# Kernel tuning notes

Measured on AMD Instinct MI355X. Metric: run time of the kernel, lower is better.

## Reference

```python
import jax, jax.numpy as jnp
import numpy as np

BLOCK_SIZE = 1024
DILATIONS = (1, 2, 4, 8)


def setup_inputs() -> dict:
    key = jax.random.key(0)
    kq, kk, kv, kw, kb = jax.random.split(key, 5)
    b, h, L, hd = 4, 8, 4096, 64
    hidden = h * hd
    return {
        "query_states": jax.random.normal(kq, (b, h, L, hd), jnp.float32),
        "key_states": jax.random.normal(kk, (b, h, L, hd), jnp.float32),
        "value_states": jax.random.normal(kv, (b, h, L, hd), jnp.float32),
        "Wo": jax.random.normal(kw, (hidden, hidden), jnp.float32),
        "bo": jax.random.normal(kb, (hidden,), jnp.float32),
    }


def _dilated_branch(q, k, v, d):
    """One dilation pass: strided gather -> block attention.
    Returns de (bsz, nh, Ld, 1) detached exp-row-sums and a (bsz, nh, Ld, hd)."""
    b, h, L, hd = q.shape
    qs, ks, vs = q[:, :, ::d], k[:, :, ::d], v[:, :, ::d]
    Ld = qs.shape[2]
    bs = min(BLOCK_SIZE, Ld)          # torch.split: one short block if Ld < block_size
    nb = Ld // bs                      # even split for chosen q_len
    blk = lambda x: x.reshape(b, h, nb, bs, hd)
    qb, kb, vb = blk(qs), blk(ks), blk(vs)
    scores = jnp.einsum('bhnqd,bhnkd->bhnqk', qb, kb) / jnp.sqrt(jnp.float32(hd))
    # detached, unstabilized exp-sum (matches attn_weights.detach().exp().sum(-1))
    de = jax.lax.stop_gradient(jnp.exp(scores).sum(-1, keepdims=True)).reshape(b, h, Ld, 1)
    probs = jax.nn.softmax(scores.astype(jnp.float32), axis=-1).astype(q.dtype)
    a = jnp.einsum('bhnqk,bhnkd->bhnqd', probs, vb).reshape(b, h, Ld, hd)
    return de, a


def reference(query_states, key_states, value_states, Wo, bo):
    b, h, L, hd = query_states.shape
    w = jnp.zeros((b, h, L, 1), jnp.float32)
    des, rs = [], []
    for d in DILATIONS:
        de, a = _dilated_branch(query_states, key_states, value_states, d)
        des.append(de)
        rs.append(a)
        w = w.at[:, :, ::d].add(de)
    out = jnp.zeros_like(query_states)
    for d, de, a in zip(DILATIONS, des, rs):
        aw = de / w[:, :, ::d]                     # (b, h, Ld, 1) relative weight
        out = out.at[:, :, ::d].add((aw * a).astype(query_states.dtype))
    out = out.transpose(0, 2, 1, 3).reshape(b, L, h * hd)
    return out @ Wo.T + bo
```

## Files before the change

### kernel.cpp

```cpp
#include <hip/hip_runtime.h>
#include <hip/hip_bf16.h>

typedef __attribute__((ext_vector_type(8))) short bf16x8;
typedef __attribute__((ext_vector_type(4))) float f32x4;
typedef unsigned short u16;

union F8 { bf16x8 v; unsigned u[4]; u16 s[8]; uint4 q; };

__device__ __forceinline__ unsigned pk2(float a, float b) {
    __hip_bfloat162 t = __float22bfloat162_rn(make_float2(a, b));
    unsigned r; __builtin_memcpy(&r, &t, 4); return r;
}
__device__ __forceinline__ u16 f2bf(float a) {
    __hip_bfloat16 t = __float2bfloat16(a);
    u16 r; __builtin_memcpy(&r, &t, 2); return r;
}
__device__ __forceinline__ float bf2f(u16 s) {
    unsigned u = ((unsigned)s) << 16; float f; __builtin_memcpy(&f, &u, 4); return f;
}
#define SWZ(byteoff, row) ((byteoff) ^ (((row) & 7) << 4))
#define MFMA(a, b, c) __builtin_amdgcn_mfma_f32_16x16x32_bf16((a), (b), (c), 0, 0, 0)

__global__ __launch_bounds__(256)
void prep_kernel(const float* __restrict__ K, const float* __restrict__ V,
                 u16* __restrict__ Kb, u16* __restrict__ Vt)
{
    __shared__ __align__(16) char tl[64 * 128];
    int blk = blockIdx.x;
    const int t = threadIdx.x;

    if (blk < 2048) {
        const int bh = blk >> 6, qt = blk & 63;
        const int q = qt * 64 + (t >> 2), dd0 = (t & 3) * 16;
        const float* kp = K + ((size_t)bh * 4096 + q) * 64 + dd0;
        float4 x0 = ((const float4*)kp)[0], x1 = ((const float4*)kp)[1];
        float4 x2 = ((const float4*)kp)[2], x3 = ((const float4*)kp)[3];
        F8 f0, f1;
        f0.u[0] = pk2(x0.x, x0.y); f0.u[1] = pk2(x0.z, x0.w);
        f0.u[2] = pk2(x1.x, x1.y); f0.u[3] = pk2(x1.z, x1.w);
        f1.u[0] = pk2(x2.x, x2.y); f1.u[1] = pk2(x2.z, x2.w);
        f1.u[2] = pk2(x3.x, x3.y); f1.u[3] = pk2(x3.z, x3.w);
        u16* op = Kb + ((size_t)bh * 4096 + q) * 64 + dd0;
        ((uint4*)op)[0] = f0.q; ((uint4*)op)[1] = f1.q;
        return;
    }
    blk -= 2048;
    int d, Ld; size_t vtoff;
    if (blk < 2048)      { d = 1; Ld = 4096; vtoff = 0; }
    else if (blk < 3072) { blk -= 2048; d = 2; Ld = 2048; vtoff = 8388608; }
    else if (blk < 3584) { blk -= 3072; d = 4; Ld = 1024; vtoff = 12582912; }
    else                 { blk -= 3584; d = 8; Ld = 512;  vtoff = 14680064; }
    const int tpb = Ld >> 6;
    const int bh = blk / tpb, jt = blk % tpb;
    {
        const int j = t >> 2, dd0 = (t & 3) * 16;
        const int q = (jt * 64 + j) * d;
        const float* vp = V + ((size_t)bh * 4096 + q) * 64 + dd0;
        float4 x0 = ((const float4*)vp)[0], x1 = ((const float4*)vp)[1];
        float4 x2 = ((const float4*)vp)[2], x3 = ((const float4*)vp)[3];
        F8 f0, f1;
        f0.u[0] = pk2(x0.x, x0.y); f0.u[1] = pk2(x0.z, x0.w);
        f0.u[2] = pk2(x1.x, x1.y); f0.u[3] = pk2(x1.z, x1.w);
        f1.u[0] = pk2(x2.x, x2.y); f1.u[1] = pk2(x2.z, x2.w);
        f1.u[2] = pk2(x3.x, x3.y); f1.u[3] = pk2(x3.z, x3.w);
        *(uint4*)(tl + SWZ(j * 128 + dd0 * 2, j)) = f0.q;
        *(uint4*)(tl + SWZ(j * 128 + dd0 * 2 + 16, j)) = f1.q;
    }
    __syncthreads();
    {
        const int dd = t >> 2, jb = (t & 3) * 16;
        F8 f0, f1;
#pragma unroll
        for (int i = 0; i < 8; ++i) {
            f0.s[i] = *(const u16*)(tl + SWZ((jb + i) * 128 + dd * 2, jb + i));
            f1.s[i] = *(const u16*)(tl + SWZ((jb + 8 + i) * 128 + dd * 2, jb + 8 + i));
        }
        u16* op = Vt + vtoff + ((size_t)bh * 64 + dd) * Ld + jt * 64 + jb;
        ((uint4*)op)[0] = f0.q; ((uint4*)op)[1] = f1.q;
    }
}

__global__ __launch_bounds__(256)
void attn_fused(const float* __restrict__ Q, const u16* __restrict__ Kb,
                const u16* __restrict__ Vt, float* __restrict__ num,
                float* __restrict__ wsum, int phase)
{
    const int L = 4096;
    const int per = gridDim.x >> 3;
    const int wg0 = blockIdx.x;
    const int wg = (wg0 & 7) * per + (wg0 >> 3);

    int d, npb, bs, rel; size_t vtoff;
    if (phase == 0)     { d = 1; npb = 32; bs = 1024; rel = wg;       vtoff = 0; }
    else if (wg < 512)  { d = 2; npb = 16; bs = 1024; rel = wg;       vtoff = 8388608; }
    else if (wg < 768)  { d = 4; npb = 8;  bs = 1024; rel = wg - 512; vtoff = 12582912; }
    else                { d = 8; npb = 4;  bs = 512;  rel = wg - 768; vtoff = 14680064; }

    const int bh = rel / npb;
    const int qt = rel % npb;
    const int b = bh >> 3, h = bh & 7;
    const int tid = threadIdx.x;
    const int w = tid >> 6, lane = tid & 63;
    const int g = lane >> 4, c = lane & 15;
    const int bstart = ((qt * 128) / bs) * bs;
    const int qrow0 = qt * 128 + w * 32;
    const int Ldq = npb * 128;
    const int nt = bs >> 6;

    __shared__ __align__(16) char smem[32 * 1024];
    char* const Kls = smem;
    char* const Vls = smem + 8192;
    char* const Pls = smem + 16384 + w * 4096;

    const size_t base = (size_t)bh * L * 64;
    const size_t vbase = vtoff + (size_t)bh * 64 * Ldq;
    const float qs = 0.125f * 1.44269504088896341f;

    bf16x8 qf[2][2];
#pragma unroll
    for (int qi = 0; qi < 2; ++qi) {
        const float* qp = Q + base + (size_t)(qrow0 + qi * 16 + c) * d * 64 + g * 8;
#pragma unroll
        for (int s2 = 0; s2 < 2; ++s2) {
            float4 x = ((const float4*)(qp + s2 * 32))[0];
            float4 y = ((const float4*)(qp + s2 * 32))[1];
            F8 f;
            f.u[0] = pk2(x.x * qs, x.y * qs);
            f.u[1] = pk2(x.z * qs, x.w * qs);
            f.u[2] = pk2(y.x * qs, y.y * qs);
            f.u[3] = pk2(y.z * qs, y.w * qs);
            qf[qi][s2] = f.v;
        }
    }

    f32x4 o[2][4];
#pragma unroll
    for (int qi = 0; qi < 2; ++qi)
#pragma unroll
        for (int dj = 0; dj < 4; ++dj) o[qi][dj] = (f32x4){0.f, 0.f, 0.f, 0.f};
    float lrow[2] = {0.f, 0.f};

    const int krow = tid >> 2, kc = tid & 3;

    uint4 ka, kb2, va, vb;
    const u16* kp0 = Kb + base + (size_t)(bstart + krow) * d * 64 + kc * 16;
    const u16* vp0 = Vt + vbase + (size_t)lane * Ldq + bstart + w * 16;
    const size_t kstep = (size_t)64 * d * 64;
    ka = ((const uint4*)kp0)[0]; kb2 = ((const uint4*)kp0)[1];
    va = ((const uint4*)vp0)[0]; vb = ((const uint4*)vp0)[1];

    for (int t = 0; t < nt; ++t) {
        *(uint4*)(Kls + SWZ(krow * 128 + kc * 32, krow)) = ka;
        *(uint4*)(Kls + SWZ(krow * 128 + kc * 32 + 16, krow)) = kb2;
        *(uint4*)(Vls + SWZ(lane * 128 + w * 32, lane)) = va;
        *(uint4*)(Vls + SWZ(lane * 128 + w * 32 + 16, lane)) = vb;
        __syncthreads();

        if (t + 1 < nt) {
            const u16* kp = kp0 + (size_t)(t + 1) * kstep;
            const u16* vp = vp0 + (t + 1) * 64;
            ka = ((const uint4*)kp)[0]; kb2 = ((const uint4*)kp)[1];
            va = ((const uint4*)vp)[0]; vb = ((const uint4*)vp)[1];
        }

        f32x4 st[2][4];
#pragma unroll
        for (int kj = 0; kj < 4; ++kj) {
            const int row = 16 * kj + c;
            bf16x8 kf0 = *(const bf16x8*)(Kls + SWZ(row * 128 + g * 16, row));
            bf16x8 kf1 = *(const bf16x8*)(Kls + SWZ(row * 128 + 64 + g * 16, row));
            f32x4 z = (f32x4){0.f, 0.f, 0.f, 0.f};
            st[0][kj] = MFMA(kf1, qf[0][1], MFMA(kf0, qf[0][0], z));
            st[1][kj] = MFMA(kf1, qf[1][1], MFMA(kf0, qf[1][0], z));
        }

#pragma unroll
        for (int qi = 0; qi < 2; ++qi) {
            const int prow = 16 * qi + c;
            float rs = 0.f;
#pragma unroll
            for (int kj = 0; kj < 4; ++kj) {
                const float p0 = exp2f(st[qi][kj][0]);
                const float p1 = exp2f(st[qi][kj][1]);
                const float p2 = exp2f(st[qi][kj][2]);
                const float p3 = exp2f(st[qi][kj][3]);
                rs += (p0 + p1) + (p2 + p3);
                uint2 pv; pv.x = pk2(p0, p1); pv.y = pk2(p2, p3);
                *(uint2*)(Pls + SWZ(prow * 128 + kj * 32 + g * 8, prow)) = pv;
            }
            lrow[qi] += rs;
        }

#pragma unroll
        for (int s = 0; s < 2; ++s) {
            bf16x8 vf[4], pf[2];
#pragma unroll
            for (int dj = 0; dj < 4; ++dj) {
                const int row = 16 * dj + c;
                vf[dj] = *(const bf16x8*)(Vls + SWZ(row * 128 + s * 64 + g * 16, row));
            }
#pragma unroll
            for (int qi = 0; qi < 2; ++qi) {
                const int row = 16 * qi + c;
                pf[qi] = *(const bf16x8*)(Pls + SWZ(row * 128 + s * 64 + g * 16, row));
            }
#pragma unroll
            for (int qi = 0; qi < 2; ++qi)
#pragma unroll
                for (int dj = 0; dj < 4; ++dj)
                    o[qi][dj] = MFMA(pf[qi], vf[dj], o[qi][dj]);
        }
        __syncthreads();
    }

#pragma unroll
    for (int qi = 0; qi < 2; ++qi) {
        float lq = lrow[qi];
        lq += __shfl_xor(lq, 16);
        lq += __shfl_xor(lq, 32);
        if (phase == 0) {
#pragma unroll
            for (int r = 0; r < 4; ++r) {
                const int q = qrow0 + 16 * qi + 4 * g + r;
                float* np = num + ((size_t)b * L + q) * 512 + h * 64 + c;
#pragma unroll
                for (int dj = 0; dj < 4; ++dj) np[dj * 16] = o[qi][dj][r];
            }
            if (g == 0) {
                const int q2 = qrow0 + 16 * qi + c;
                wsum[((size_t)b * L + q2) * 8 + h] = lq;
            }
        } else {
#pragma unroll
            for (int r = 0; r < 4; ++r) {
                const int q = qrow0 + 16 * qi + 4 * g + r;
                float* np = num + ((size_t)b * L + (size_t)q * d) * 512 + h * 64 + c;
#pragma unroll
                for (int dj = 0; dj < 4; ++dj)
                    atomicAdd(np + dj * 16, o[qi][dj][r]);
            }
            if (g == 0) {
                const int q2 = qrow0 + 16 * qi + c;
                atomicAdd(wsum + ((size_t)b * L + (size_t)q2 * d) * 8 + h, lq);
            }
        }
    }
}

__global__ __launch_bounds__(256)
void proj_mfma(const float* __restrict__ num, const float* __restrict__ wsum,
               const float* __restrict__ Wo, const float* __restrict__ bo,
               float* __restrict__ out)
{
    __shared__ __align__(16) char smem[64 * 1024];
    char* const Ah = smem;
    char* const Al = smem + 16384;
    char* const Bh = smem + 32768;
    char* const Bl = smem + 49152;

    const int tid = threadIdx.x;
    const int w = tid >> 6, lane = tid & 63, g = lane >> 4, c = lane & 15;
    const int wm = (w >> 1) * 64, wn = (w & 1) * 64;
    const int per = gridDim.x >> 3;
    const int wg0 = blockIdx.x;
    const int wg = (wg0 & 7) * per + (wg0 >> 3);
    const int bm = (wg >> 2) * 128, bn = (wg & 3) * 128;
    const int srow = tid >> 1, koff = (tid & 1) * 32;

    f32x4 acc[4][4];
#pragma unroll
    for (int mi = 0; mi < 4; ++mi)
#pragma unroll
        for (int ni = 0; ni < 4; ++ni) acc[mi][ni] = (f32x4){0.f, 0.f, 0.f, 0.f};

    for (int bk = 0; bk < 512; bk += 64) {
        {
            const float* ap = num + (size_t)(bm + srow) * 512 + bk + koff;
            const float winv = 1.0f / wsum[(size_t)(bm + srow) * 8 + (bk >> 6)];
#pragma unroll
            for (int i = 0; i < 8; ++i) {
                float4 a4 = ((const float4*)ap)[i];
                float v0 = a4.x * winv, v1 = a4.y * winv, v2 = a4.z * winv, v3 = a4.w * winv;
                u16 h0 = f2bf(v0), h1 = f2bf(v1), h2 = f2bf(v2), h3 = f2bf(v3);
                uint2 hiw; hiw.x = h0 | ((unsigned)h1 << 16); hiw.y = h2 | ((unsigned)h3 << 16);
                uint2 lo;
                lo.x = f2bf(v0 - bf2f(h0)) | ((unsigned)f2bf(v1 - bf2f(h1)) << 16);
                lo.y = f2bf(v2 - bf2f(h2)) | ((unsigned)f2bf(v3 - bf2f(h3)) << 16);
                const int off = SWZ(srow * 128 + koff * 2 + i * 8, srow);
                *(uint2*)(Ah + off) = hiw;
                *(uint2*)(Al + off) = lo;
            }
            const float* bp = Wo + (size_t)(bn + srow) * 512 + bk + koff;
#pragma unroll
            for (int i = 0; i < 8; ++i) {
                float4 a4 = ((const float4*)bp)[i];
                u16 h0 = f2bf(a4.x), h1 = f2bf(a4.y), h2 = f2bf(a4.z), h3 = f2bf(a4.w);
                uint2 hiw; hiw.x = h0 | ((unsigned)h1 << 16); hiw.y = h2 | ((unsigned)h3 << 16);
                uint2 lo;
                lo.x = f2bf(a4.x - bf2f(h0)) | ((unsigned)f2bf(a4.y - bf2f(h1)) << 16);
                lo.y = f2bf(a4.z - bf2f(h2)) | ((unsigned)f2bf(a4.w - bf2f(h3)) << 16);
                const int off = SWZ(srow * 128 + koff * 2 + i * 8, srow);
                *(uint2*)(Bh + off) = hiw;
                *(uint2*)(Bl + off) = lo;
            }
        }
        __syncthreads();
#pragma unroll
        for (int s = 0; s < 2; ++s) {
            bf16x8 ah[4], al[4], bh[4], bl[4];
#pragma unroll
            for (int mi = 0; mi < 4; ++mi) {
                const int row = wm + 16 * mi + c;
                const int off = SWZ(row * 128 + s * 64 + g * 16, row);
                ah[mi] = *(const bf16x8*)(Ah + off);
                al[mi] = *(const bf16x8*)(Al + off);
            }
#pragma unroll
            for (int ni = 0; ni < 4; ++ni) {
                const int row = wn + 16 * ni + c;
                const int off = SWZ(row * 128 + s * 64 + g * 16, row);
                bh[ni] = *(const bf16x8*)(Bh + off);
                bl[ni] = *(const bf16x8*)(Bl + off);
            }
#pragma unroll
            for (int mi = 0; mi < 4; ++mi)
#pragma unroll
                for (int ni = 0; ni < 4; ++ni) {
                    acc[mi][ni] = MFMA(ah[mi], bh[ni], acc[mi][ni]);
                    acc[mi][ni] = MFMA(ah[mi], bl[ni], acc[mi][ni]);
                    acc[mi][ni] = MFMA(al[mi], bh[ni], acc[mi][ni]);
                }
        }
        __syncthreads();
    }

    float bias[4];
#pragma unroll
    for (int ni = 0; ni < 4; ++ni) bias[ni] = bo[bn + wn + 16 * ni + c];
#pragma unroll
    for (int mi = 0; mi < 4; ++mi)
#pragma unroll
        for (int r = 0; r < 4; ++r) {
            float* op = out + (size_t)(bm + wm + 16 * mi + 4 * g + r) * 512 + bn + wn + c;
#pragma unroll
            for (int ni = 0; ni < 4; ++ni)
                op[ni * 16] = acc[mi][ni][r] + bias[ni];
        }
}

extern "C" void kernel_launch(void* const* d_in, const int* in_sizes, int n_in,
                              void* d_out, int out_size, void* d_ws, size_t ws_size,
                              hipStream_t stream)
{
    const float* Q  = (const float*)d_in[0];
    const float* K  = (const float*)d_in[1];
    const float* V  = (const float*)d_in[2];
    const float* Wo = (const float*)d_in[3];
    const float* bo = (const float*)d_in[4];
    float* out = (float*)d_out;

    float* num  = (float*)d_ws;
    float* wsum = num + (size_t)8388608;
    u16*  Kb    = (u16*)((char*)d_ws + 34078720);
    u16*  Vt    = (u16*)((char*)d_ws + 50855936);

    hipLaunchKernelGGL(prep_kernel, dim3(5888), dim3(256), 0, stream, K, V, Kb, Vt);
    hipLaunchKernelGGL(attn_fused, dim3(1024), dim3(256), 0, stream,
                       Q, Kb, Vt, num, wsum, 0);
    hipLaunchKernelGGL(attn_fused, dim3(896), dim3(256), 0, stream,
                       Q, Kb, Vt, num, wsum, 1);
    hipLaunchKernelGGL(proj_mfma, dim3(512), dim3(256), 0, stream,
                       num, wsum, Wo, bo, out);
}
```

Measured before the change: 207.8 us.

## Keep softmax probabilities in registers by permuting V key order in prep

Instead of writing exponentiated scores to shared memory and reading them back as MFMA A-operands, the probabilities are packed directly from the score accumulator registers into bf16x8 fragments. To make the register layout match, the V-transpose prep kernel permutes the key index within each 64-key tile. This removes the P shared-memory round trip and halves LDS use, which may raise occupancy. In exchange it couples the V layout to the MFMA output layout, which must be exactly right for correctness.

```diff
diff --git a/kernel.cpp b/kernel.cpp
--- a/kernel.cpp
+++ b/kernel.cpp
@@ -17,6 +17,9 @@
 }
 __device__ __forceinline__ float bf2f(u16 s) {
     unsigned u = ((unsigned)s) << 16; float f; __builtin_memcpy(&f, &u, 4); return f;
+}
+__device__ __forceinline__ int vperm(int p) {
+    return 32 * (p >> 5) + 16 * ((p >> 2) & 1) + 4 * ((p >> 3) & 3) + (p & 3);
 }
 #define SWZ(byteoff, row) ((byteoff) ^ (((row) & 7) << 4))
 #define MFMA(a, b, c) __builtin_amdgcn_mfma_f32_16x16x32_bf16((a), (b), (c), 0, 0, 0)
@@ -72,8 +75,9 @@
         F8 f0, f1;
 #pragma unroll
         for (int i = 0; i < 8; ++i) {
-            f0.s[i] = *(const u16*)(tl + SWZ((jb + i) * 128 + dd * 2, jb + i));
-            f1.s[i] = *(const u16*)(tl + SWZ((jb + 8 + i) * 128 + dd * 2, jb + 8 + i));
+            const int k0 = vperm(jb + i), k1 = vperm(jb + 8 + i);
+            f0.s[i] = *(const u16*)(tl + SWZ(k0 * 128 + dd * 2, k0));
+            f1.s[i] = *(const u16*)(tl + SWZ(k1 * 128 + dd * 2, k1));
         }
         u16* op = Vt + vtoff + ((size_t)bh * 64 + dd) * Ld + jt * 64 + jb;
         ((uint4*)op)[0] = f0.q; ((uint4*)op)[1] = f1.q;
@@ -107,10 +111,9 @@
     const int Ldq = npb * 128;
     const int nt = bs >> 6;
 
-    __shared__ __align__(16) char smem[32 * 1024];
+    __shared__ __align__(16) char smem[16 * 1024];
     char* const Kls = smem;
     char* const Vls = smem + 8192;
-    char* const Pls = smem + 16384 + w * 4096;
 
     const size_t base = (size_t)bh * L * 64;
     const size_t vbase = vtoff + (size_t)bh * 64 * Ldq;
@@ -174,41 +177,43 @@
             st[1][kj] = MFMA(kf1, qf[1][1], MFMA(kf0, qf[1][0], z));
         }
 
+        bf16x8 pa[2][2];
 #pragma unroll
         for (int qi = 0; qi < 2; ++qi) {
-            const int prow = 16 * qi + c;
+            float p[4][4];
             float rs = 0.f;
 #pragma unroll
-            for (int kj = 0; kj < 4; ++kj) {
-                const float p0 = exp2f(st[qi][kj][0]);
-                const float p1 = exp2f(st[qi][kj][1]);
-                const float p2 = exp2f(st[qi][kj][2]);
-                const float p3 = exp2f(st[qi][kj][3]);
-                rs += (p0 + p1) + (p2 + p3);
-                uint2 pv; pv.x = pk2(p0, p1); pv.y = pk2(p2, p3);
-                *(uint2*)(Pls + SWZ(prow * 128 + kj * 32 + g * 8, prow)) = pv;
-            }
+            for (int kj = 0; kj < 4; ++kj)
+#pragma unroll
+                for (int r = 0; r < 4; ++r) {
+                    p[kj][r] = exp2f(st[qi][kj][r]);
+                    rs += p[kj][r];
+                }
             lrow[qi] += rs;
+#pragma unroll
+            for (int s = 0; s < 2; ++s) {
+                F8 f;
+                f.u[0] = pk2(p[2 * s][0], p[2 * s][1]);
+                f.u[1] = pk2(p[2 * s][2], p[2 * s][3]);
+                f.u[2] = pk2(p[2 * s + 1][0], p[2 * s + 1][1]);
+                f.u[3] = pk2(p[2 * s + 1][2], p[2 * s + 1][3]);
+                pa[qi][s] = f.v;
+            }
         }
 
 #pragma unroll
         for (int s = 0; s < 2; ++s) {
-            bf16x8 vf[4], pf[2];
+            bf16x8 vf[4];
 #pragma unroll
             for (int dj = 0; dj < 4; ++dj) {
                 const int row = 16 * dj + c;
                 vf[dj] = *(const bf16x8*)(Vls + SWZ(row * 128 + s * 64 + g * 16, row));
             }
 #pragma unroll
-            for (int qi = 0; qi < 2; ++qi) {
-                const int row = 16 * qi + c;
-                pf[qi] = *(const bf16x8*)(Pls + SWZ(row * 128 + s * 64 + g * 16, row));
-            }
-#pragma unroll
             for (int qi = 0; qi < 2; ++qi)
 #pragma unroll
                 for (int dj = 0; dj < 4; ++dj)
-                    o[qi][dj] = MFMA(pf[qi], vf[dj], o[qi][dj]);
+                    o[qi][dj] = MFMA(pa[qi][s], vf[dj], o[qi][dj]);
         }
         __syncthreads();
     }
```

After: 214.8 us. 1.03x slower.
